# Kernel tuning notes

Measured on AMD Instinct MI355X. Metric: run time of the kernel, lower is better.

The kernel has to match this reference:

```python
import jax, jax.numpy as jnp
import numpy as np

B, T, IN, H, OUT = 4096, 512, 4, 64, 1


def setup_inputs() -> dict:
    key = jax.random.key(0)
    ks = jax.random.split(key, 12)
    s_in = 1.0 / np.sqrt(H)
    u = lambda k, shape: jax.random.uniform(k, shape, jnp.float32, -s_in, s_in)
    return {
        "x": jax.random.normal(ks[0], (B, T, IN), jnp.float32),
        "W_ih0": u(ks[1], (4 * H, IN)),
        "W_hh0": u(ks[2], (4 * H, H)),
        "b_ih0": u(ks[3], (4 * H,)),
        "b_hh0": u(ks[4], (4 * H,)),
        "W_ih1": u(ks[5], (4 * H, H)),
        "W_hh1": u(ks[6], (4 * H, H)),
        "b_ih1": u(ks[7], (4 * H,)),
        "b_hh1": u(ks[8], (4 * H,)),
        "W_fc": u(ks[9], (OUT, H)),
        "b_fc": u(ks[10], (OUT,)),
    }


def _lstm_layer(x_seq, W_ih, W_hh, b_ih, b_hh):
    # x_seq: [B, T, D]. PyTorch gate order: i, f, g, o.
    # Precompute input projection for all timesteps (one big GEMM).
    x_proj = jnp.einsum("btd,gd->btg", x_seq, W_ih) + b_ih + b_hh  # [B, T, 4H]
    x_proj = jnp.swapaxes(x_proj, 0, 1)  # [T, B, 4H]
    Bsz = x_seq.shape[0]
    h0 = jnp.zeros((Bsz, W_hh.shape[1]), x_seq.dtype)
    c0 = jnp.zeros_like(h0)

    def step(carry, xp):
        h, c = carry
        gates = xp + h @ W_hh.T  # [B, 4H]
        i, f, g, o = jnp.split(gates, 4, axis=-1)
        i = jax.nn.sigmoid(i)
        f = jax.nn.sigmoid(f)
        g = jnp.tanh(g)
        o = jax.nn.sigmoid(o)
        c_new = f * c + i * g
        h_new = o * jnp.tanh(c_new)
        return (h_new, c_new), h_new

    (hT, cT), h_seq = jax.lax.scan(step, (h0, c0), x_proj)
    return jnp.swapaxes(h_seq, 0, 1), hT  # [B, T, H], [B, H]


def reference(x, W_ih0, W_hh0, b_ih0, b_hh0, W_ih1, W_hh1, b_ih1, b_hh1, W_fc, b_fc):
    h1_seq, _ = _lstm_layer(x, W_ih0, W_hh0, b_ih0, b_hh0)
    _, h2_last = _lstm_layer(h1_seq, W_ih1, W_hh1, b_ih1, b_hh1)
    return h2_last @ W_fc.T + b_fc  # [B, 1]
```

## Files before the change

kernel.cpp:

```cpp
#include <hip/hip_runtime.h>

#define TSEQ 512
#define NTH  512

typedef __attribute__((ext_vector_type(8))) _Float16 half8;
typedef __attribute__((ext_vector_type(4))) float f32x4;
typedef __attribute__((ext_vector_type(4))) unsigned int u32x4;

__device__ __forceinline__ unsigned packF16x2(float a, float b) {
    _Float16 ha = (_Float16)a, hb = (_Float16)b;
    unsigned short ua = __builtin_bit_cast(unsigned short, ha);
    unsigned short ub = __builtin_bit_cast(unsigned short, hb);
    return (unsigned)ua | ((unsigned)ub << 16);
}
__device__ __forceinline__ half8 packA16(const float w8[8]) {
    u32x4 W = { packF16x2(w8[0], w8[1]), packF16x2(w8[2], w8[3]),
                packF16x2(w8[4], w8[5]), packF16x2(w8[6], w8[7]) };
    return __builtin_bit_cast(half8, W);
}

#define MFMA(a, b, c) __builtin_amdgcn_mfma_f32_16x16x32_f16((a), (b), (c), 0, 0, 0)
#define LD128H(p) __builtin_bit_cast(half8, *(const u32x4*)(p))

__device__ __forceinline__ float act_fused(float ai, float af, float ag, float ao, float* c) {
    const float L2E = 1.44269504088896340736f;
    float ei = __builtin_amdgcn_exp2f(-ai * L2E);
    float ef = __builtin_amdgcn_exp2f(-af * L2E);
    float eg = __builtin_amdgcn_exp2f(2.0f * L2E * ag);
    float eo = __builtin_amdgcn_exp2f(-ao * L2E);
    float sf = __builtin_amdgcn_rcpf(1.0f + ef);
    float ig = (eg - 1.0f) * __builtin_amdgcn_rcpf((1.0f + ei) * (eg + 1.0f));
    float cn = fmaf(*c, sf, ig);
    *c = cn;
    float ec = __builtin_amdgcn_exp2f(2.0f * L2E * cn);
    return (ec - 1.0f) * __builtin_amdgcn_rcpf((1.0f + eo) * (ec + 1.0f));
}

__global__ __launch_bounds__(NTH, 2)
void lstm2_mfma(const float* __restrict__ x,
                const float* __restrict__ W_ih0, const float* __restrict__ W_hh0,
                const float* __restrict__ b_ih0, const float* __restrict__ b_hh0,
                const float* __restrict__ W_ih1, const float* __restrict__ W_hh1,
                const float* __restrict__ b_ih1, const float* __restrict__ b_hh1,
                const float* __restrict__ W_fc,  const float* __restrict__ b_fc,
                float* __restrict__ out)
{
    const int tid  = threadIdx.x;
    const int lane = tid & 63;
    const int wv   = tid >> 6;
    const int rl   = lane & 15;
    const int g    = lane >> 4;
    const int b0   = blockIdx.x * 16;

    __shared__ unsigned h0P0[512], h0P1[512];
    __shared__ unsigned h1P0[512], h1P1[512];
    __shared__ float fcl[64 * 17];

    for (int i2 = tid; i2 < 512; i2 += NTH) {
        h0P0[i2] = 0u; h0P1[i2] = 0u; h1P0[i2] = 0u; h1P1[i2] = 0u;
    }
    __syncthreads();

    const int offL = rl*32 + (((g + rl) & 7) << 2);
    const int offH = rl*32 + (((4 + g + rl) & 7) << 2);
    const int q0w  = 8*((wv & 3)) + 2*g;
    const int woff = rl*32 + ((((q0w >> 2) + rl) & 7) << 2) + (q0w & 3);

    if (wv < 4) {
        const int w = wv;
        half8 A0[4][2];
        half8 Ax[4];
        f32x4 bias4[4];
        #pragma unroll
        for (int G = 0; G < 4; ++G) {
            const int row = 64*G + 16*w + rl;
            #pragma unroll
            for (int s = 0; s < 2; ++s) {
                float w8[8];
                const float* src = W_hh0 + row*64 + s*32 + g*8;
                #pragma unroll
                for (int e = 0; e < 8; ++e) w8[e] = src[e];
                A0[G][s] = packA16(w8);
            }
            {
                u32x4 ax = {0u, 0u, 0u, 0u};
                if (g == 0) {
                    ax.x = packF16x2(W_ih0[row*4+0], W_ih0[row*4+1]);
                    ax.y = packF16x2(W_ih0[row*4+2], W_ih0[row*4+3]);
                }
                Ax[G] = __builtin_bit_cast(half8, ax);
            }
            const int rb = 64*G + 16*w + 4*g;
            bias4[G].x = b_ih0[rb+0] + b_hh0[rb+0];
            bias4[G].y = b_ih0[rb+1] + b_hh0[rb+1];
            bias4[G].z = b_ih0[rb+2] + b_hh0[rb+2];
            bias4[G].w = b_ih0[rb+3] + b_hh0[rb+3];
        }
        float cst[4] = {0.f, 0.f, 0.f, 0.f};

        f32x4 xcur = *(const f32x4*)(x + ((size_t)(b0 + rl) * TSEQ) * 4);

        auto body0 = [&](const unsigned* rP, unsigned* wP, int i) {
            half8 B0 = LD128H(rP + offL);
            half8 B1 = LD128H(rP + offH);
            u32x4 tx = {0u, 0u, 0u, 0u};
            if (g == 0) {
                tx.x = packF16x2(xcur.x, xcur.y);
                tx.y = packF16x2(xcur.z, xcur.w);
            }
            half8 Bx = __builtin_bit_cast(half8, tx);

            f32x4 acc[4];
            __builtin_amdgcn_s_setprio(1);
            #pragma unroll
            for (int G = 0; G < 4; ++G) acc[G] = MFMA(Ax[G], Bx, bias4[G]);
            #pragma unroll
            for (int G = 0; G < 4; ++G) acc[G] = MFMA(A0[G][0], B0, acc[G]);
            #pragma unroll
            for (int G = 0; G < 4; ++G) acc[G] = MFMA(A0[G][1], B1, acc[G]);
            __builtin_amdgcn_s_setprio(0);

            float hv[4];
            #pragma unroll
            for (int j = 0; j < 4; ++j)
                hv[j] = act_fused(acc[0][j], acc[1][j], acc[2][j], acc[3][j], &cst[j]);
            *(uint2*)(wP + woff) = make_uint2(packF16x2(hv[0], hv[1]),
                                              packF16x2(hv[2], hv[3]));

            if (i + 1 < TSEQ)
                xcur = *(const f32x4*)(x + ((size_t)(b0 + rl) * TSEQ + (i + 1)) * 4);
        };

        for (int ii = 0; ii < 256; ++ii) {
            body0(h0P0, h0P1, 2*ii);     __syncthreads();
            body0(h0P1, h0P0, 2*ii + 1); __syncthreads();
        }
        __syncthreads();
        __syncthreads();
    } else {
        const int w = wv - 4;
        half8 A1[4][4];
        f32x4 bias4[4];
        #pragma unroll
        for (int G = 0; G < 4; ++G) {
            const int row = 64*G + 16*w + rl;
            #pragma unroll
            for (int s = 0; s < 4; ++s) {
                float w8[8];
                const float* src = (s < 2) ? (W_ih1 + row*64 + s*32 + g*8)
                                           : (W_hh1 + row*64 + (s-2)*32 + g*8);
                #pragma unroll
                for (int e = 0; e < 8; ++e) w8[e] = src[e];
                A1[G][s] = packA16(w8);
            }
            const int rb = 64*G + 16*w + 4*g;
            bias4[G].x = b_ih1[rb+0] + b_hh1[rb+0];
            bias4[G].y = b_ih1[rb+1] + b_hh1[rb+1];
            bias4[G].z = b_ih1[rb+2] + b_hh1[rb+2];
            bias4[G].w = b_ih1[rb+3] + b_hh1[rb+3];
        }
        float cst[4] = {0.f, 0.f, 0.f, 0.f};
        const int u0 = 16*w + 4*g;

        half8 pB0 = {}, pB1 = {};

        auto body1 = [&](const unsigned* r1P,
                         unsigned* wP,
                         const unsigned* n0P,
                         bool wrFC) {
            half8 B2 = LD128H(r1P + offL);
            half8 B3 = LD128H(r1P + offH);

            f32x4 acc[4];
            __builtin_amdgcn_s_setprio(1);
            #pragma unroll
            for (int G = 0; G < 4; ++G) acc[G] = MFMA(A1[G][0], pB0, bias4[G]);
            #pragma unroll
            for (int G = 0; G < 4; ++G) acc[G] = MFMA(A1[G][1], pB1, acc[G]);
            #pragma unroll
            for (int G = 0; G < 4; ++G) acc[G] = MFMA(A1[G][2], B2, acc[G]);
            #pragma unroll
            for (int G = 0; G < 4; ++G) acc[G] = MFMA(A1[G][3], B3, acc[G]);
            __builtin_amdgcn_s_setprio(0);

            pB0 = LD128H(n0P + offL);
            pB1 = LD128H(n0P + offH);

            float hv[4];
            #pragma unroll
            for (int j = 0; j < 4; ++j)
                hv[j] = act_fused(acc[0][j], acc[1][j], acc[2][j], acc[3][j], &cst[j]);
            *(uint2*)(wP + woff) = make_uint2(packF16x2(hv[0], hv[1]),
                                              packF16x2(hv[2], hv[3]));
            if (wrFC) {
                #pragma unroll
                for (int j = 0; j < 4; ++j) fcl[(u0 + j)*17 + rl] = hv[j];
            }
        };

        __syncthreads();
        pB0 = LD128H(h0P1 + offL);
        pB1 = LD128H(h0P1 + offH);
        __syncthreads();
        for (int ii = 0; ii < 256; ++ii) {
            body1(h1P0, h1P1, h0P0, false);     __syncthreads();
            body1(h1P1, h1P0, h0P1, ii == 255); __syncthreads();
        }
    }

    if (tid < 16) {
        float acc = b_fc[0];
        #pragma unroll 16
        for (int u = 0; u < 64; ++u) acc += fcl[u*17 + tid] * W_fc[u];
        out[b0 + tid] = acc;
    }
}

extern "C" void kernel_launch(void* const* d_in, const int* in_sizes, int n_in,
                              void* d_out, int out_size, void* d_ws, size_t ws_size,
                              hipStream_t stream) {
    const float* x     = (const float*)d_in[0];
    const float* W_ih0 = (const float*)d_in[1];
    const float* W_hh0 = (const float*)d_in[2];
    const float* b_ih0 = (const float*)d_in[3];
    const float* b_hh0 = (const float*)d_in[4];
    const float* W_ih1 = (const float*)d_in[5];
    const float* W_hh1 = (const float*)d_in[6];
    const float* b_ih1 = (const float*)d_in[7];
    const float* b_hh1 = (const float*)d_in[8];
    const float* W_fc  = (const float*)d_in[9];
    const float* b_fc  = (const float*)d_in[10];
    float* out = (float*)d_out;

    dim3 grid(4096 / 16), block(NTH);
    hipLaunchKernelGGL(lstm2_mfma, grid, block, 0, stream,
                       x, W_ih0, W_hh0, b_ih0, b_hh0,
                       W_ih1, W_hh1, b_ih1, b_hh1, W_fc, b_fc, out);
}
```

Measured before the change: 372.2 us.

## Fold activation exponent scales into weights and prefetch x earlier

Pre-scales the weight rows and biases by -log2(e), or 2·log2(e) for the g gate, when packing to fp16. The MFMA outputs can then feed exp2 directly, removing a multiply per gate per step on the serial critical path. The x load for the next step is issued at the start of the step and packed after the activations, hiding global load latency. Launch bounds also change from 2 to 1 blocks per CU. Scaling the fp16 weights slightly changes rounding, and the occupancy hint change may alter register allocation.

```diff
diff --git a/kernel.cpp b/kernel.cpp
--- a/kernel.cpp
+++ b/kernel.cpp
@@ -13,9 +13,9 @@
     unsigned short ub = __builtin_bit_cast(unsigned short, hb);
     return (unsigned)ua | ((unsigned)ub << 16);
 }
-__device__ __forceinline__ half8 packA16(const float w8[8]) {
-    u32x4 W = { packF16x2(w8[0], w8[1]), packF16x2(w8[2], w8[3]),
-                packF16x2(w8[4], w8[5]), packF16x2(w8[6], w8[7]) };
+__device__ __forceinline__ half8 packA16s(const float w8[8], float s) {
+    u32x4 W = { packF16x2(w8[0]*s, w8[1]*s), packF16x2(w8[2]*s, w8[3]*s),
+                packF16x2(w8[4]*s, w8[5]*s), packF16x2(w8[6]*s, w8[7]*s) };
     return __builtin_bit_cast(half8, W);
 }
 
@@ -23,20 +23,20 @@
 #define LD128H(p) __builtin_bit_cast(half8, *(const u32x4*)(p))
 
 __device__ __forceinline__ float act_fused(float ai, float af, float ag, float ao, float* c) {
-    const float L2E = 1.44269504088896340736f;
-    float ei = __builtin_amdgcn_exp2f(-ai * L2E);
-    float ef = __builtin_amdgcn_exp2f(-af * L2E);
-    float eg = __builtin_amdgcn_exp2f(2.0f * L2E * ag);
-    float eo = __builtin_amdgcn_exp2f(-ao * L2E);
+    const float L2E2 = 2.88539008177792681472f;
+    float ei = __builtin_amdgcn_exp2f(ai);
+    float ef = __builtin_amdgcn_exp2f(af);
+    float eg = __builtin_amdgcn_exp2f(ag);
+    float eo = __builtin_amdgcn_exp2f(ao);
     float sf = __builtin_amdgcn_rcpf(1.0f + ef);
     float ig = (eg - 1.0f) * __builtin_amdgcn_rcpf((1.0f + ei) * (eg + 1.0f));
     float cn = fmaf(*c, sf, ig);
     *c = cn;
-    float ec = __builtin_amdgcn_exp2f(2.0f * L2E * cn);
+    float ec = __builtin_amdgcn_exp2f(cn * L2E2);
     return (ec - 1.0f) * __builtin_amdgcn_rcpf((1.0f + eo) * (ec + 1.0f));
 }
 
-__global__ __launch_bounds__(NTH, 2)
+__global__ __launch_bounds__(NTH, 1)
 void lstm2_mfma(const float* __restrict__ x,
                 const float* __restrict__ W_ih0, const float* __restrict__ W_hh0,
                 const float* __restrict__ b_ih0, const float* __restrict__ b_hh0,
@@ -52,6 +52,9 @@
     const int g    = lane >> 4;
     const int b0   = blockIdx.x * 16;
 
+    const float NL2E = -1.44269504088896340736f;
+    const float PL2E2 = 2.88539008177792681472f;
+
     __shared__ unsigned h0P0[512], h0P1[512];
     __shared__ unsigned h1P0[512], h1P1[512];
     __shared__ float fcl[64 * 17];
@@ -73,6 +76,7 @@
         f32x4 bias4[4];
         #pragma unroll
         for (int G = 0; G < 4; ++G) {
+            const float sc = (G == 2) ? PL2E2 : NL2E;
             const int row = 64*G + 16*w + rl;
             #pragma unroll
             for (int s = 0; s < 2; ++s) {
@@ -80,34 +84,36 @@
                 const float* src = W_hh0 + row*64 + s*32 + g*8;
                 #pragma unroll
                 for (int e = 0; e < 8; ++e) w8[e] = src[e];
-                A0[G][s] = packA16(w8);
+                A0[G][s] = packA16s(w8, sc);
             }
             {
                 u32x4 ax = {0u, 0u, 0u, 0u};
                 if (g == 0) {
-                    ax.x = packF16x2(W_ih0[row*4+0], W_ih0[row*4+1]);
-                    ax.y = packF16x2(W_ih0[row*4+2], W_ih0[row*4+3]);
+                    ax.x = packF16x2(W_ih0[row*4+0]*sc, W_ih0[row*4+1]*sc);
+                    ax.y = packF16x2(W_ih0[row*4+2]*sc, W_ih0[row*4+3]*sc);
                 }
                 Ax[G] = __builtin_bit_cast(half8, ax);
             }
             const int rb = 64*G + 16*w + 4*g;
-            bias4[G].x = b_ih0[rb+0] + b_hh0[rb+0];
-            bias4[G].y = b_ih0[rb+1] + b_hh0[rb+1];
-            bias4[G].z = b_ih0[rb+2] + b_hh0[rb+2];
-            bias4[G].w = b_ih0[rb+3] + b_hh0[rb+3];
+            bias4[G].x = (b_ih0[rb+0] + b_hh0[rb+0]) * sc;
+            bias4[G].y = (b_ih0[rb+1] + b_hh0[rb+1]) * sc;
+            bias4[G].z = (b_ih0[rb+2] + b_hh0[rb+2]) * sc;
+            bias4[G].w = (b_ih0[rb+3] + b_hh0[rb+3]) * sc;
         }
         float cst[4] = {0.f, 0.f, 0.f, 0.f};
 
-        f32x4 xcur = *(const f32x4*)(x + ((size_t)(b0 + rl) * TSEQ) * 4);
+        f32x4 xf = *(const f32x4*)(x + ((size_t)(b0 + rl) * TSEQ) * 4);
+        unsigned bx0 = packF16x2(xf.x, xf.y);
+        unsigned bx1 = packF16x2(xf.z, xf.w);
 
         auto body0 = [&](const unsigned* rP, unsigned* wP, int i) {
+            if (i + 1 < TSEQ)
+                xf = *(const f32x4*)(x + ((size_t)(b0 + rl) * TSEQ + (i + 1)) * 4);
+
             half8 B0 = LD128H(rP + offL);
             half8 B1 = LD128H(rP + offH);
             u32x4 tx = {0u, 0u, 0u, 0u};
-            if (g == 0) {
-                tx.x = packF16x2(xcur.x, xcur.y);
-                tx.y = packF16x2(xcur.z, xcur.w);
-            }
+            if (g == 0) { tx.x = bx0; tx.y = bx1; }
             half8 Bx = __builtin_bit_cast(half8, tx);
 
             f32x4 acc[4];
@@ -124,11 +130,12 @@
             #pragma unroll
             for (int j = 0; j < 4; ++j)
                 hv[j] = act_fused(acc[0][j], acc[1][j], acc[2][j], acc[3][j], &cst[j]);
+
+            bx0 = packF16x2(xf.x, xf.y);
+            bx1 = packF16x2(xf.z, xf.w);
+
             *(uint2*)(wP + woff) = make_uint2(packF16x2(hv[0], hv[1]),
                                               packF16x2(hv[2], hv[3]));
-
-            if (i + 1 < TSEQ)
-                xcur = *(const f32x4*)(x + ((size_t)(b0 + rl) * TSEQ + (i + 1)) * 4);
         };
 
         for (int ii = 0; ii < 256; ++ii) {
@@ -143,6 +150,7 @@
         f32x4 bias4[4];
         #pragma unroll
         for (int G = 0; G < 4; ++G) {
+            const float sc = (G == 2) ? PL2E2 : NL2E;
             const int row = 64*G + 16*w + rl;
             #pragma unroll
             for (int s = 0; s < 4; ++s) {
@@ -151,13 +159,13 @@
                                            : (W_hh1 + row*64 + (s-2)*32 + g*8);
                 #pragma unroll
                 for (int e = 0; e < 8; ++e) w8[e] = src[e];
-                A1[G][s] = packA16(w8);
+                A1[G][s] = packA16s(w8, sc);
             }
             const int rb = 64*G + 16*w + 4*g;
-            bias4[G].x = b_ih1[rb+0] + b_hh1[rb+0];
-            bias4[G].y = b_ih1[rb+1] + b_hh1[rb+1];
-            bias4[G].z = b_ih1[rb+2] + b_hh1[rb+2];
-            bias4[G].w = b_ih1[rb+3] + b_hh1[rb+3];
+            bias4[G].x = (b_ih1[rb+0] + b_hh1[rb+0]) * sc;
+            bias4[G].y = (b_ih1[rb+1] + b_hh1[rb+1]) * sc;
+            bias4[G].z = (b_ih1[rb+2] + b_hh1[rb+2]) * sc;
+            bias4[G].w = (b_ih1[rb+3] + b_hh1[rb+3]) * sc;
         }
         float cst[4] = {0.f, 0.f, 0.f, 0.f};
         const int u0 = 16*w + 4*g;
```

After: 341.7 us. 8.2% less time.
